# Kernel optimization log

Measured on AMD Instinct MI355X. Metric: run time of the kernel, lower is better.

## Reference

```python
import jax, jax.numpy as jnp
import numpy as np

OUTLINER_RATIO = 0.01
RANK = 16
SVD_NITER = 2  # matches torch.svd_lowrank default


def _randomized_svd(A, rank, key, niter=SVD_NITER):
    # torch.svd_lowrank-style randomized range finder + small SVD.
    n, d = A.shape
    Omega = jax.random.normal(key, (d, rank), dtype=A.dtype)
    Q, _ = jnp.linalg.qr(A @ Omega)               # [n, rank]
    for _ in range(niter):
        Q, _ = jnp.linalg.qr(A.T @ Q)             # [d, rank]
        Q, _ = jnp.linalg.qr(A @ Q)               # [n, rank]
    B = Q.T @ A                                   # [rank, d]
    Ub, S, Vh = jnp.linalg.svd(B, full_matrices=False)
    U = Q @ Ub                                    # [n, rank]
    return U, S, Vh


def get_statistics(x, outliner_ratio):
    # threshold such that ~outliner_ratio fraction of |x| exceeds it
    return jnp.quantile(jnp.abs(x), 1.0 - outliner_ratio)


def compress(x, outliner, rank, key):
    # split outliers (kept exactly) from sub-outlier part (low-rank compressed)
    x_outlier = jnp.where(jnp.abs(x) > outliner, x, jnp.zeros((), x.dtype))
    x_sub = (x - x_outlier).reshape(-1, x.shape[-1])   # [N, D]
    U, S, Vh = _randomized_svd(x_sub, rank, key)
    R = Vh.T                                           # [D, rank]
    Rinv = Vh                                          # orthonormal -> pinv = transpose
    L = x_sub @ R                                      # [N, rank]
    return x_outlier, L, R, Rinv


def reference(x, iteration):
    result = jax.nn.silu(x)
    # iteration < 10 branch: compute fresh outlier statistics
    outliner = get_statistics(x, OUTLINER_RATIO)
    # iteration % 50 == 0 -> execute_svd = True (iteration = 0 here)
    key = jax.random.key(42)
    x_outlier_compressed, L, R, Rinv = compress(x, outliner, RANK, key)
    return result, outliner, R, Rinv


def setup_inputs() -> dict:
    key = jax.random.key(0)
    x = jax.random.normal(key, (4, 2048, 4096), dtype=jnp.float32)
    return {"x": x, "iteration": 0}
```

## Files before the change

### kernel.cpp

```cpp
#include <hip/hip_runtime.h>
#include <math.h>


#define N_TOTAL 33554432
#define DDIM    4096
#define NROWS   8192
#define NCHUNK  32
#define RTARGET 33218888u

__device__ __forceinline__ double frcp(double x){
  double r = (double)(1.0f/(float)x);
  r = r*(2.0 - x*r);
  r = r*(2.0 - x*r);
  return r;
}
__device__ __forceinline__ double frsqrt(double x){
  double r = (double)rsqrtf((float)x);
  double hx = 0.5*x;
  r = r*(1.5 - hx*r*r);
  r = r*(1.5 - hx*r*r);
  return r;
}
__device__ __forceinline__ double fsqrt(double x){
  return (x == 0.0) ? 0.0 : x*frsqrt(x);
}
__device__ __forceinline__ double frcp1(double x){
  double r = (double)(1.0f/(float)x);
  r = r*(2.0 - x*r);
  return r;
}
__device__ __forceinline__ double frsqrt1(double x){
  double r = (double)rsqrtf((float)x);
  r = r*(1.5 - (0.5*x)*r*r);
  return r;
}
__device__ __forceinline__ double fsqrt1(double x){
  return (x == 0.0) ? 0.0 : x*frsqrt1(x);
}

__device__ __forceinline__ double dsign(double a, double b){ return (b >= 0.0) ? fabs(a) : -fabs(a); }

__device__ __forceinline__ void f_slartg(double f, double g, double& c, double& s, double& r){
  if (g == 0.0){ c=1.0; s=0.0; r=f; }
  else if (f == 0.0){ c=0.0; s=dsign(1.0,g); r=fabs(g); }
  else {
    double d2 = f*f+g*g;
    double inv = frsqrt1(d2);
    c = fabs(f)*inv;
    r = dsign(d2*inv, f);
    s = g*inv*dsign(1.0,f);
  }
}

__device__ void f_slas2(double f, double g, double h, double& ssmin, double& ssmax){
  double fa=fabs(f), ga=fabs(g), ha=fabs(h);
  double fhmn=fmin(fa,ha), fhmx=fmax(fa,ha);
  if (fhmn == 0.0){
    ssmin=0.0;
    if (fhmx==0.0) ssmax=ga;
    else { double mx=fmax(fhmx,ga), mn=fmin(fhmx,ga); double q=mn*frcp1(mx); ssmax = mx*fsqrt1(1.0+q*q); }
  } else {
    if (ga < fhmx){
      double rinv = frcp1(fhmx);
      double as_=1.0+fhmn*rinv, at=(fhmx-fhmn)*rinv, au=ga*rinv; au=au*au;
      double c=2.0*frcp1(fsqrt1(as_*as_+au)+fsqrt1(at*at+au));
      ssmin=fhmn*c; ssmax=fhmx*frcp1(c);
    } else {
      double au=fhmx*frcp1(ga);
      if (au==0.0){ ssmin=(fhmn*fhmx)*frcp1(ga); ssmax=ga; }
      else {
        double rinv = frcp1(fhmx);
        double as_=1.0+fhmn*rinv, at=(fhmx-fhmn)*rinv;
        double c=frcp1(fsqrt1(1.0+(as_*au)*(as_*au))+fsqrt1(1.0+(at*au)*(at*au)));
        ssmin=(fhmn*c)*au; ssmin=ssmin+ssmin; ssmax=ga*frcp1(c+c);
      }
    }
  }
}

__device__ void f_slasv2(double f, double g, double h,
                         double& ssmin, double& ssmax, double& snr, double& csr, double& snl, double& csl){
  const double EPSd = 5.9604645e-8;
  double ft=f, fa=fabs(f), ht=h, ha=fabs(h);
  int pmax=1;
  bool swap_=(ha>fa);
  if (swap_){ pmax=3; double t=ft; ft=ht; ht=t; t=fa; fa=ha; ha=t; }
  double gt=g, ga=fabs(g);
  double clt=0, crt=0, slt=0, srt=0;
  if (ga == 0.0){ ssmin=ha; ssmax=fa; clt=1; crt=1; slt=0; srt=0; }
  else {
    bool gasmal=true;
    if (ga > fa){
      pmax=2;
      if ((fa*frcp1(ga)) < EPSd){
        gasmal=false;
        ssmax=ga;
        ssmin = (ha>1.0) ? (fa*frcp1(ga*frcp1(ha))) : ((fa*frcp1(ga))*ha);
        clt=1; slt=ht*frcp1(gt); srt=1; crt=ft*frcp1(gt);
      }
    }
    if (gasmal){
      double d_=fa-ha;
      double fainv = frcp1(fa);
      double l_=(d_==fa)?1.0:(d_*fainv);
      double m_=gt*frcp1(ft);
      double t_=2.0-l_;
      double mm=m_*m_, tt=t_*t_;
      double s_=fsqrt1(tt+mm);
      double r_=(l_==0.0)?fabs(m_):fsqrt1(l_*l_+mm);
      double a_=0.5*(s_+r_);
      double ainv = frcp1(a_);
      ssmin=ha*ainv;
      ssmax=fa*a_;
      if (mm==0.0){
        t_=(l_==0.0)?(dsign(2.0,ft)*dsign(1.0,gt)):(gt*frcp1(dsign(d_,ft))+m_*frcp1(t_));
      } else {
        t_=(m_*frcp1(s_+t_)+m_*frcp1(r_+l_))*(1.0+a_);
      }
      l_=fsqrt1(t_*t_+4.0);
      double linv = frcp1(l_);
      crt=2.0*linv;
      srt=t_*linv;
      clt=(crt+srt*m_)*ainv;
      slt=(ht*frcp1(ft))*srt*ainv;
    }
  }
  if (swap_){ csl=srt; snl=crt; csr=slt; snr=clt; }
  else { csl=clt; snl=slt; csr=crt; snr=srt; }
  double tsign=0.0;
  if (pmax==1) tsign = dsign(1.0,csr)*dsign(1.0,csl)*dsign(1.0,f);
  if (pmax==2) tsign = dsign(1.0,snr)*dsign(1.0,csl)*dsign(1.0,g);
  if (pmax==3) tsign = dsign(1.0,snr)*dsign(1.0,snl)*dsign(1.0,h);
  ssmax = dsign(ssmax, tsign);
  ssmin = dsign(ssmin, tsign*dsign(1.0,f)*dsign(1.0,h));
}

__global__ __launch_bounds__(256) void k_hist1(const float4* __restrict__ x4, unsigned* __restrict__ h1){
  __shared__ unsigned lh[4096];
  for (int i=threadIdx.x; i<4096; i+=256) lh[i]=0u;
  __syncthreads();
  int tid = blockIdx.x*blockDim.x + threadIdx.x;
  int stride = gridDim.x*blockDim.x;
  for (int i = tid; i < N_TOTAL/4; i += stride){
    float4 v = x4[i];
    atomicAdd(&lh[(__float_as_uint(v.x)&0x7FFFFFFFu)>>19], 1u);
    atomicAdd(&lh[(__float_as_uint(v.y)&0x7FFFFFFFu)>>19], 1u);
    atomicAdd(&lh[(__float_as_uint(v.z)&0x7FFFFFFFu)>>19], 1u);
    atomicAdd(&lh[(__float_as_uint(v.w)&0x7FFFFFFFu)>>19], 1u);
  }
  __syncthreads();
  for (int i=threadIdx.x; i<4096; i+=256){ unsigned c=lh[i]; if (c) atomicAdd(&h1[i], c); }
}

__global__ __launch_bounds__(256) void k_siluhist(const float4* __restrict__ x4, float4* __restrict__ o4,
                                                  unsigned* __restrict__ h1){
  __shared__ unsigned lh[4096];
  for (int i=threadIdx.x; i<4096; i+=256) lh[i]=0u;
  __syncthreads();
  int tid = blockIdx.x*blockDim.x + threadIdx.x;
  int stride = gridDim.x*blockDim.x;
  for (int i = tid; i < N_TOTAL/4; i += stride){
    float4 v = x4[i];
    float4 o;
    o.x = v.x / (1.0f + expf(-v.x));
    o.y = v.y / (1.0f + expf(-v.y));
    o.z = v.z / (1.0f + expf(-v.z));
    o.w = v.w / (1.0f + expf(-v.w));
    o4[i] = o;
    atomicAdd(&lh[(__float_as_uint(v.x)&0x7FFFFFFFu)>>19], 1u);
    atomicAdd(&lh[(__float_as_uint(v.y)&0x7FFFFFFFu)>>19], 1u);
    atomicAdd(&lh[(__float_as_uint(v.z)&0x7FFFFFFFu)>>19], 1u);
    atomicAdd(&lh[(__float_as_uint(v.w)&0x7FFFFFFFu)>>19], 1u);
  }
  __syncthreads();
  for (int i=threadIdx.x; i<4096; i+=256){ unsigned c=lh[i]; if (c) atomicAdd(&h1[i], c); }
}

__global__ __launch_bounds__(1024) void k_select1(const unsigned* __restrict__ h1, unsigned* __restrict__ sel){
  __shared__ unsigned ssum[1024];
  int t = threadIdx.x;
  unsigned psum = 0;
  for (int k=0;k<4;++k) psum += h1[t*4+k];
  ssum[t]=psum; __syncthreads();
  for (int off=1; off<1024; off<<=1){
    unsigned v = (t>=off)? ssum[t-off]:0u;
    __syncthreads();
    ssum[t] += v;
    __syncthreads();
  }
  unsigned incl = ssum[t], excl = incl - psum;
  if (excl <= RTARGET && RTARGET < incl){
    unsigned run = excl;
    for (int k=0;k<4;++k){
      unsigned c = h1[t*4+k];
      if (run + c > RTARGET){ sel[1]=(unsigned)(t*4+k); sel[2]=RTARGET-run; break; }
      run += c;
    }
  }
}

__global__ void k_hist2(const float4* __restrict__ x4, unsigned* __restrict__ h2, const unsigned* __restrict__ sel){
  unsigned hstar = sel[1];
  int tid = blockIdx.x*blockDim.x + threadIdx.x;
  int stride = gridDim.x*blockDim.x;
  for (int i = tid; i < N_TOTAL/4; i += stride){
    float4 v = x4[i];
    unsigned b;
    b = __float_as_uint(v.x) & 0x7FFFFFFFu; if ((b>>19)==hstar) atomicAdd(&h2[b&0x7FFFFu],1u);
    b = __float_as_uint(v.y) & 0x7FFFFFFFu; if ((b>>19)==hstar) atomicAdd(&h2[b&0x7FFFFu],1u);
    b = __float_as_uint(v.z) & 0x7FFFFFFFu; if ((b>>19)==hstar) atomicAdd(&h2[b&0x7FFFFu],1u);
    b = __float_as_uint(v.w) & 0x7FFFFFFFu; if ((b>>19)==hstar) atomicAdd(&h2[b&0x7FFFFu],1u);
  }
}

__global__ __launch_bounds__(128) void k_grpsum(const uint4* __restrict__ h2v, unsigned* __restrict__ gs){
  __shared__ unsigned red[128];
  int g = blockIdx.x, t = threadIdx.x;
  uint4 v = h2v[(size_t)g*128 + t];
  red[t] = v.x+v.y+v.z+v.w;
  __syncthreads();
  for (int off=64; off; off>>=1){ if (t<off) red[t] += red[t+off]; __syncthreads(); }
  if (t==0) gs[g] = red[0];
}

__global__ __launch_bounds__(1024) void k_select2b(const unsigned* __restrict__ gs, const unsigned* __restrict__ h2,
                                                   unsigned* __restrict__ sel, float* __restrict__ outScalar){
  __shared__ unsigned ssum[1024];
  __shared__ unsigned sg[2];
  int t = threadIdx.x;
  unsigned target = sel[2], hstar = sel[1];
  unsigned psum = gs[t];
  ssum[t]=psum; __syncthreads();
  for (int off=1; off<1024; off<<=1){
    unsigned v = (t>=off)? ssum[t-off]:0u;
    __syncthreads();
    ssum[t] += v;
    __syncthreads();
  }
  unsigned incl = ssum[t], excl = incl - psum;
  if (excl <= target && target < incl){ sg[0]=(unsigned)t; sg[1]=excl; }
  __syncthreads();
  unsigned g = sg[0], gexcl = sg[1];
  unsigned cnt = (t<512) ? h2[(size_t)g*512 + t] : 0u;
  __syncthreads();
  ssum[t]=cnt; __syncthreads();
  for (int off=1; off<1024; off<<=1){
    unsigned v = (t>=off)? ssum[t-off]:0u;
    __syncthreads();
    ssum[t] += v;
    __syncthreads();
  }
  unsigned incl2 = ssum[t], excl2 = incl2 - cnt;
  unsigned rem = target - gexcl;
  if (t < 512 && excl2 <= rem && rem < incl2){
    unsigned tb = (hstar<<19) | (g*512 + (unsigned)t);
    float tv = __uint_as_float(tb);
    ((float*)sel)[0] = tv;
    *outScalar = tv;
  }
}

__device__ __forceinline__ unsigned rotl32(unsigned x, int r){ return (x<<r)|(x>>(32-r)); }

__device__ __forceinline__ float bits_to_normal(unsigned g){
  float u01 = __uint_as_float((g>>9) | 0x3F800000u) - 1.0f;
  float u = __fadd_rn(__fmul_rn(u01, 2.0f), -0.99999994f);
  u = fmaxf(-0.99999994f, u);
  float xx = __fmul_rn(u,u);
  float w = -log1pf(-xx);
  float p;
  if (w < 5.0f){
    w = __fadd_rn(w, -2.5f);
    p = 2.81022636e-08f;
    p = __fadd_rn(3.43273939e-07f, __fmul_rn(p,w));
    p = __fadd_rn(-3.5233877e-06f, __fmul_rn(p,w));
    p = __fadd_rn(-4.39150654e-06f, __fmul_rn(p,w));
    p = __fadd_rn(0.00021858087f, __fmul_rn(p,w));
    p = __fadd_rn(-0.00125372503f, __fmul_rn(p,w));
    p = __fadd_rn(-0.00417768164f, __fmul_rn(p,w));
    p = __fadd_rn(0.246640727f, __fmul_rn(p,w));
    p = __fadd_rn(1.50140941f, __fmul_rn(p,w));
  } else {
    w = __fadd_rn(sqrtf(w), -3.0f);
    p = -0.000200214257f;
    p = __fadd_rn(0.000100950558f, __fmul_rn(p,w));
    p = __fadd_rn(0.00134934322f, __fmul_rn(p,w));
    p = __fadd_rn(-0.00367342844f, __fmul_rn(p,w));
    p = __fadd_rn(0.00573950773f, __fmul_rn(p,w));
    p = __fadd_rn(-0.0076224613f, __fmul_rn(p,w));
    p = __fadd_rn(0.00943887047f, __fmul_rn(p,w));
    p = __fadd_rn(1.00167406f, __fmul_rn(p,w));
    p = __fadd_rn(2.83297682f, __fmul_rn(p,w));
  }
  return __fmul_rn(__uint_as_float(0x3FB504F3u), __fmul_rn(p,u));
}

#define TF_ROUND(r) { x0 += x1; x1 = rotl32(x1,(r)); x1 ^= x0; }

__global__ void k_omega(float* __restrict__ om){
  unsigned p = blockIdx.x*blockDim.x + threadIdx.x;
  unsigned x0 = p, x1 = 32768u + p;
  const unsigned ks0 = 0u, ks1 = 42u, ks2 = 0x1BD11BDAu ^ 0u ^ 42u;
  x0 += ks0; x1 += ks1;
  TF_ROUND(13) TF_ROUND(15) TF_ROUND(26) TF_ROUND(6)   x0+=ks1; x1+=ks2+1u;
  TF_ROUND(17) TF_ROUND(29) TF_ROUND(16) TF_ROUND(24)  x0+=ks2; x1+=ks0+2u;
  TF_ROUND(13) TF_ROUND(15) TF_ROUND(26) TF_ROUND(6)   x0+=ks0; x1+=ks1+3u;
  TF_ROUND(17) TF_ROUND(29) TF_ROUND(16) TF_ROUND(24)  x0+=ks1; x1+=ks2+4u;
  TF_ROUND(13) TF_ROUND(15) TF_ROUND(26) TF_ROUND(6)   x0+=ks2; x1+=ks0+5u;
  om[p]         = bits_to_normal(x0);
  om[p+32768u]  = bits_to_normal(x1);
}

__global__ __launch_bounds__(256) void k_gemmA(const float* __restrict__ x, const float* __restrict__ W,
                                               float* __restrict__ Y, const float* __restrict__ sel){
  __shared__ float xs[16][128];
  __shared__ float ws[128][16];
  const float t = sel[0];
  const int tid = threadIdx.x;
  const int c = tid & 15, rl = tid >> 4;
  const int row0 = blockIdx.x*16;
  const int c8 = c*8;
  const int wk = (tid*8) >> 4, wc = (tid*8) & 15;
  double acc = 0.0;
  for (int kt = 0; kt < DDIM; kt += 128){
    const float4* p = (const float4*)(x + (size_t)(row0+rl)*DDIM + kt + c8);
    float4 a = p[0], b = p[1];
    xs[rl][c8+0] = (fabsf(a.x) > t) ? 0.0f : a.x;
    xs[rl][c8+1] = (fabsf(a.y) > t) ? 0.0f : a.y;
    xs[rl][c8+2] = (fabsf(a.z) > t) ? 0.0f : a.z;
    xs[rl][c8+3] = (fabsf(a.w) > t) ? 0.0f : a.w;
    xs[rl][c8+4] = (fabsf(b.x) > t) ? 0.0f : b.x;
    xs[rl][c8+5] = (fabsf(b.y) > t) ? 0.0f : b.y;
    xs[rl][c8+6] = (fabsf(b.z) > t) ? 0.0f : b.z;
    xs[rl][c8+7] = (fabsf(b.w) > t) ? 0.0f : b.w;
    const float4* q = (const float4*)(W + (size_t)kt*16 + tid*8);
    float4 wa = q[0], wb = q[1];
    float* dstw = &ws[wk][wc];
    dstw[0]=wa.x; dstw[1]=wa.y; dstw[2]=wa.z; dstw[3]=wa.w;
    dstw[4]=wb.x; dstw[5]=wb.y; dstw[6]=wb.z; dstw[7]=wb.w;
    __syncthreads();
    #pragma unroll
    for (int k=0;k<128;k+=2){
      float2 xv2 = *(const float2*)&xs[rl][k];
      acc += (double)xv2.x*(double)ws[k][c];
      acc += (double)xv2.y*(double)ws[k+1][c];
    }
    __syncthreads();
  }
  Y[(size_t)(row0+rl)*16 + c] = (float)acc;
}

__global__ __launch_bounds__(256) void k_gemmAT(const float* __restrict__ x, const float* __restrict__ Q,
                                                double* __restrict__ part, const float* __restrict__ sel){
  __shared__ float qs[128][16];
  const float t = sel[0];
  const int tid = threadIdx.x;
  const int d = blockIdx.x*256 + tid;
  const int chunk = blockIdx.y;
  const int i0 = chunk*(NROWS/NCHUNK);
  double acc[16];
  #pragma unroll
  for (int c=0;c<16;++c) acc[c]=0.0;
  for (int it=0; it<NROWS/NCHUNK; it+=128){
    if (tid < 128){
      const float4* src = (const float4*)(Q + (size_t)(i0+it)*16) + tid*4;
      float4 a = src[0], b = src[1], c4 = src[2], d4 = src[3];
      float* dst = &qs[0][0] + tid*16;
      dst[0]=a.x; dst[1]=a.y; dst[2]=a.z; dst[3]=a.w;
      dst[4]=b.x; dst[5]=b.y; dst[6]=b.z; dst[7]=b.w;
      dst[8]=c4.x; dst[9]=c4.y; dst[10]=c4.z; dst[11]=c4.w;
      dst[12]=d4.x; dst[13]=d4.y; dst[14]=d4.z; dst[15]=d4.w;
    }
    __syncthreads();
    for (int ii=0; ii<128; ++ii){
      float xv = x[(size_t)(i0+it+ii)*DDIM + d];
      xv = (fabsf(xv) > t) ? 0.0f : xv;
      double xd = (double)xv;
      #pragma unroll
      for (int c2=0;c2<8;++c2){
        float2 q2 = *(const float2*)&qs[ii][c2*2];
        acc[c2*2]   += xd*(double)q2.x;
        acc[c2*2+1] += xd*(double)q2.y;
      }
    }
    __syncthreads();
  }
  double* pp = part + ((size_t)chunk*DDIM + d)*16;
  #pragma unroll
  for (int c=0;c<16;++c) pp[c]=acc[c];
}

__global__ void k_reduceT(const double* __restrict__ part, float* __restrict__ outM, int asB, int nchunks){
  int idx = blockIdx.x*blockDim.x + threadIdx.x;
  if (idx >= DDIM*16) return;
  double s = 0.0;
  for (int c=0;c<nchunks;++c) s += part[(size_t)c*DDIM*16 + idx];
  int d = idx >> 4, r = idx & 15;
  if (asB) outM[(size_t)r*DDIM + d] = (float)s;
  else     outM[idx] = (float)s;
}

__device__ void redchol_body(const double* part, int nchunks, double* Lout, double* Uinv,
                             double (*Gs)[17], double (*Vs)[17], int t){
  {
    double s = 0.0;
    for (int c=0;c<nchunks;++c) s += part[(size_t)c*256 + t];
    Gs[t>>4][t&15] = s;
  }
  __syncthreads();
  int l = t;
  for (int k=0;k<16;++k){
    if (l==k) Gs[k][k] = fsqrt(Gs[k][k]);
    __syncthreads();
    if (l>k && l<16) Gs[k][l] = Gs[k][l]*frcp(Gs[k][k]);
    __syncthreads();
    if (l>k && l<16){
      double g = Gs[k][l];
      for (int i=k+1;i<=l;++i) Gs[i][l] -= Gs[k][i]*g;
    }
    __syncthreads();
  }
  if (l<16){
    for (int i=0;i<16;++i) Vs[i][l] = 0.0;
    Vs[l][l] = frcp(Gs[l][l]);
    for (int i=l-1;i>=0;--i){
      double s = 0.0;
      for (int k=i+1;k<=l;++k) s += Gs[i][k]*Vs[k][l];
      Vs[i][l] = -s*frcp(Gs[i][i]);
    }
  }
  __syncthreads();
  if (l<16){
    for (int c=0;c<16;++c){
      Lout[l*16+c] = (c<=l) ? Gs[c][l] : 0.0;
      Uinv[l*16+c] = (l<=c) ? Vs[l][c] : 0.0;
    }
  }
}

__global__ __launch_bounds__(256) void k_gramMC(const float* __restrict__ M, int rowsPerChunk,
                                                double* __restrict__ part,
                                                double* __restrict__ Lout, double* __restrict__ Uinv,
                                                unsigned* __restrict__ ctr){
  __shared__ float lds[16][17];
  __shared__ double Gs[16][17];
  __shared__ double Vs[16][17];
  __shared__ unsigned slast;
  int t = threadIdx.x; int i = t>>4, j = t&15;
  int r0 = blockIdx.x*rowsPerChunk;
  double acc = 0.0;
  for (int rt=0; rt<rowsPerChunk; rt+=16){
    lds[t>>4][t&15] = M[(size_t)(r0+rt+(t>>4))*16 + (t&15)];
    __syncthreads();
    #pragma unroll
    for (int dd2=0; dd2<16; ++dd2) acc += (double)lds[dd2][i]*(double)lds[dd2][j];
    __syncthreads();
  }
  part[(size_t)blockIdx.x*256 + t] = acc;
  __threadfence();
  if (t==0) slast = atomicAdd(ctr, 1u);
  __syncthreads();
  if (slast != gridDim.x-1u) return;
  __threadfence();
  redchol_body(part, (int)gridDim.x, Lout, Uinv, Gs, Vs, t);
  __syncthreads();
  if (t==0) *ctr = 0u;
}

__global__ __launch_bounds__(256) void k_gramBC(const float* __restrict__ B,
                                                double* __restrict__ part,
                                                double* __restrict__ Lout, double* __restrict__ Uinv,
                                                unsigned* __restrict__ ctr){
  __shared__ float lds[16][17];
  __shared__ double Gs[16][17];
  __shared__ double Vs[16][17];
  __shared__ unsigned slast;
  int t = threadIdx.x; int i = t>>4, j = t&15;
  int d0 = blockIdx.x*256;
  double acc = 0.0;
  for (int dt=0; dt<256; dt+=16){
    lds[t>>4][t&15] = B[(size_t)(t>>4)*DDIM + d0+dt+(t&15)];
    __syncthreads();
    #pragma unroll
    for (int dd2=0; dd2<16; ++dd2) acc += (double)lds[i][dd2]*(double)lds[j][dd2];
    __syncthreads();
  }
  part[(size_t)blockIdx.x*256 + t] = acc;
  __threadfence();
  if (t==0) slast = atomicAdd(ctr, 1u);
  __syncthreads();
  if (slast != gridDim.x-1u) return;
  __threadfence();
  redchol_body(part, (int)gridDim.x, Lout, Uinv, Gs, Vs, t);
  __syncthreads();
  if (t==0) *ctr = 0u;
}

__global__ __launch_bounds__(256) void k_applyRinv(float* __restrict__ M, const double* __restrict__ Uinv){
  __shared__ double su[256];
  int t = threadIdx.x;
  su[t] = Uinv[t];
  int r = blockIdx.x*16 + (t>>4);
  int j = t & 15;
  const float4* rp = (const float4*)(M + (size_t)r*16);
  float4 v0=rp[0], v1=rp[1], v2=rp[2], v3=rp[3];
  float rowv[16] = {v0.x,v0.y,v0.z,v0.w, v1.x,v1.y,v1.z,v1.w,
                    v2.x,v2.y,v2.z,v2.w, v3.x,v3.y,v3.z,v3.w};
  __syncthreads();
  double acc = 0.0;
  #pragma unroll
  for (int k=0;k<16;++k) acc += (double)rowv[k]*su[k*16+j];
  M[(size_t)r*16 + j] = (float)acc;
}

__global__ __launch_bounds__(64) void k_smallsvd(const double* __restrict__ Lg, double* __restrict__ Wout){
  __shared__ double Lm[16][16];
  __shared__ double VT[16][16];
  __shared__ double A1[16][16];
  __shared__ double dd[16], ee[16], tp[16];
  __shared__ double csv[16], snv[16];
  int l = threadIdx.x;
  for (int idx=l; idx<256; idx+=64){ int r=idx>>4, c=idx&15; Lm[r][c] = (c<=r)? Lg[r*16+c] : 0.0; }
  __syncthreads();
  for (int i=0;i<16;++i){
    double xn2=0.0;
    for (int r=i+1;r<16;++r){ double v=Lm[r][i]; xn2 += v*v; }
    double alpha = Lm[i][i];
    double beta, tauq_, scl;
    if (xn2==0.0){ tauq_=0.0; beta=alpha; scl=0.0; }
    else { beta = -dsign(fsqrt1(alpha*alpha+xn2), alpha); tauq_=(beta-alpha)*frcp1(beta); scl=frcp1(alpha-beta); }
    __syncthreads();
    if (l>i && l<16) Lm[l][i] *= scl;
    __syncthreads();
    dd[i]=beta;
    if (tauq_ != 0.0 && l>i && l<16){
      int j=l;
      double w = Lm[i][j];
      for (int r=i+1;r<16;++r) w += Lm[r][i]*Lm[r][j];
      w *= tauq_;
      Lm[i][j] -= w;
      for (int r=i+1;r<16;++r) Lm[r][j] -= w*Lm[r][i];
    }
    __syncthreads();
    if (i<15){
      double xn2b=0.0;
      for (int c=i+2;c<16;++c){ double v=Lm[i][c]; xn2b+=v*v; }
      double alpha2=Lm[i][i+1];
      double beta2, taup_, scl2;
      if (xn2b==0.0){ taup_=0.0; beta2=alpha2; scl2=0.0; }
      else { beta2=-dsign(fsqrt1(alpha2*alpha2+xn2b),alpha2); taup_=(beta2-alpha2)*frcp1(beta2); scl2=frcp1(alpha2-beta2); }
      __syncthreads();
      if (l>=i+2 && l<16) Lm[i][l] *= scl2;
      __syncthreads();
      ee[i]=beta2; tp[i]=taup_;
      if (taup_!=0.0 && l>i && l<16){
        int r=l;
        double w=Lm[r][i+1];
        for (int c=i+2;c<16;++c) w += Lm[i][c]*Lm[r][c];
        w *= taup_;
        Lm[r][i+1] -= w;
        for (int c=i+2;c<16;++c) Lm[r][c] -= w*Lm[i][c];
      }
      __syncthreads();
    } else { tp[i]=0.0; __syncthreads(); }
  }
  for (int idx=l; idx<256; idx+=64){ int r=idx>>4,c=idx&15; VT[r][c]=(r==c)?1.0:0.0; }
  __syncthreads();
  const double EPSs = 5.9604645e-8;
  const double UNFL = 1.17549435e-38;
  double tol = 10.0*EPSs;
  double sminoa, mu;
  sminoa = mu = fabs(dd[0]);
  if (sminoa != 0.0){
    for (int k=1;k<16;++k){ mu = fabs(dd[k])*(mu*frcp1(mu+fabs(ee[k-1]))); sminoa=fmin(sminoa,mu); if (sminoa==0.0) break; }
  }
  sminoa = sminoa/4.0;
  double thresh = fmax(tol*sminoa, 6.0*16.0*16.0*UNFL);
  int m=16, oldll=-1, oldm=-1, idir=0;
  double sminl=0.0;
  int guard=0;
  #define Dv(k) dd[(k)-1]
  #define Ev(k) ee[(k)-1]
  while (m > 1 && guard < 3000){
    ++guard;
    int ll=0; bool split=false;
    double smax_=fabs(Dv(m)), smin_=smax_;
    for (int lll=1; lll<=m-1; ++lll){
      ll = m-lll;
      double abss=fabs(Dv(ll)), abse=fabs(Ev(ll));
      if (abse <= thresh){ split=true; break; }
      smin_=fmin(smin_,abss); smax_=fmax(smax_,fmax(abss,abse));
    }
    if (!split) ll=0;
    else {
      Ev(ll)=0.0;
      if (ll == m-1){ m = m-1; continue; }
    }
    ll = ll+1;
    if (ll == m-1){
      double sigmn,sigmx,sinr,cosr,sinl_,cosl;
      f_slasv2(Dv(m-1), Ev(m-1), Dv(m), sigmn, sigmx, sinr, cosr, sinl_, cosl);
      Dv(m-1)=sigmx; Ev(m-1)=0.0; Dv(m)=sigmn;
      if (l<16){
        double t0 = cosr*VT[m-2][l] + sinr*VT[m-1][l];
        VT[m-1][l] = cosr*VT[m-1][l] - sinr*VT[m-2][l];
        VT[m-2][l] = t0;
      }
      __syncthreads();
      m -= 2; continue;
    }
    if (ll > oldm || m < oldll) idir = (fabs(Dv(ll)) >= fabs(Dv(m))) ? 1 : 2;
    bool cont=false;
    if (idir==1){
      if (fabs(Ev(m-1)) <= tol*fabs(Dv(m))){ Ev(m-1)=0.0; continue; }
      mu = fabs(Dv(ll)); sminl=mu;
      for (int lll=ll; lll<=m-1; ++lll){
        if (fabs(Ev(lll)) <= tol*mu){ Ev(lll)=0.0; cont=true; break; }
        mu = fabs(Dv(lll+1))*(mu*frcp1(mu+fabs(Ev(lll)))); sminl=fmin(sminl,mu);
      }
    } else {
      if (fabs(Ev(ll)) <= tol*fabs(Dv(ll))){ Ev(ll)=0.0; continue; }
      mu = fabs(Dv(m)); sminl=mu;
      for (int lll=m-1; lll>=ll; --lll){
        if (fabs(Ev(lll)) <= tol*mu){ Ev(lll)=0.0; cont=true; break; }
        mu = fabs(Dv(lll))*(mu*frcp1(mu+fabs(Ev(lll)))); sminl=fmin(sminl,mu);
      }
    }
    if (cont) continue;
    oldll=ll; oldm=m;
    double shift=0.0, rdum;
    if (!( 16.0*tol*(sminl*frcp1(smax_)) <= fmax(EPSs, 0.01*tol) )){
      double sll;
      if (idir==1){ sll=fabs(Dv(ll)); f_slas2(Dv(m-1), Ev(m-1), Dv(m), shift, rdum); }
      else        { sll=fabs(Dv(m));  f_slas2(Dv(ll), Ev(ll), Dv(ll+1), shift, rdum); }
      if (sll>0.0){ double q=shift*frcp1(sll); if (q*q < EPSs) shift=0.0; }
    }
    if (shift == 0.0){
      if (idir==1){
        double cs=1.0, oldcs=1.0, oldsn=0.0, r_;
        double dcur = Dv(ll);
        for (int i1=ll;i1<=m-1;++i1){
          double cn, snn;
          double a0 = dcur*cs;
          f_slartg(a0, Ev(i1), cn, snn, r_);
          if (i1>ll) Ev(i1-1) = oldsn*r_;
          double dnx = Dv(i1+1);
          double ocn, osn, dnew;
          f_slartg(oldcs*r_, dnx*snn, ocn, osn, dnew);
          Dv(i1)=dnew;
          cs=cn; oldcs=ocn; oldsn=osn;
          csv[i1-1]=cs; snv[i1-1]=snn;
          dcur = dnx;
        }
        double h=dcur*cs;
        Dv(m)=h*oldcs; Ev(m-1)=h*oldsn;
        if (fabs(Ev(m-1))<=thresh) Ev(m-1)=0.0;
        __syncthreads();
        if (l<16){
          double v = VT[ll-1][l];
          for (int i1=ll;i1<=m-1;++i1){
            double c=csv[i1-1], s=snv[i1-1];
            double w = VT[i1][l];
            VT[i1-1][l] = c*v + s*w;
            v = c*w - s*v;
          }
          VT[m-1][l] = v;
        }
      } else {
        double cs=1.0, oldcs=1.0, oldsn=0.0, r_;
        double dcur = Dv(m);
        for (int i1=m;i1>=ll+1;--i1){
          double cn,snn;
          double a0 = dcur*cs;
          f_slartg(a0, Ev(i1-1), cn, snn, r_);
          if (i1<m) Ev(i1)=oldsn*r_;
          double dnx = Dv(i1-1);
          double ocn,osn,dnew;
          f_slartg(oldcs*r_, dnx*snn, ocn, osn, dnew);
          Dv(i1)=dnew;
          cs=cn; oldcs=ocn; oldsn=osn;
          csv[i1-2]=oldcs; snv[i1-2]=-oldsn;
          dcur = dnx;
        }
        double h=dcur*cs;
        Dv(ll)=h*oldcs; Ev(ll)=h*oldsn;
        if (fabs(Ev(ll))<=thresh) Ev(ll)=0.0;
        __syncthreads();
        if (l<16){
          double v = VT[m-1][l];
          for (int i1=m;i1>=ll+1;--i1){
            double c=csv[i1-2], s=snv[i1-2];
            double w = VT[i1-2][l];
            VT[i1-1][l] = c*v - s*w;
            v = c*w + s*v;
          }
          VT[ll-1][l] = v;
        }
      }
    } else {
      if (idir==1){
        double f=(fabs(Dv(ll))-shift)*(dsign(1.0,Dv(ll))+shift*frcp1(Dv(ll)));
        double g=Ev(ll);
        double dcur = Dv(ll), ecur = Ev(ll);
        double r_;
        for (int i1=ll;i1<=m-1;++i1){
          double cosr,sinr,cosl,sinl_;
          double dnx = Dv(i1+1);
          f_slartg(f,g,cosr,sinr,r_);
          if (i1>ll) Ev(i1-1)=r_;
          f = cosr*dcur + sinr*ecur;
          double e_mid = cosr*ecur - sinr*dcur;
          g = sinr*dnx;
          double d_mid = cosr*dnx;
          f_slartg(f,g,cosl,sinl_,r_);
          Dv(i1)=r_;
          f = cosl*e_mid + sinl_*d_mid;
          double d_fin = cosl*d_mid - sinl_*e_mid;
          double e_fin = 0.0;
          if (i1 < m-1){ double enx = Ev(i1+1); g = sinl_*enx; e_fin = cosl*enx; }
          csv[i1-1]=cosr; snv[i1-1]=sinr;
          dcur = d_fin; ecur = e_fin;
        }
        Dv(m) = dcur;
        Ev(m-1)=f;
        if (fabs(Ev(m-1))<=thresh) Ev(m-1)=0.0;
        __syncthreads();
        if (l<16){
          double v = VT[ll-1][l];
          for (int i1=ll;i1<=m-1;++i1){
            double c=csv[i1-1], s=snv[i1-1];
            double w = VT[i1][l];
            VT[i1-1][l] = c*v + s*w;
            v = c*w - s*v;
          }
          VT[m-1][l] = v;
        }
      } else {
        double f=(fabs(Dv(m))-shift)*(dsign(1.0,Dv(m))+shift*frcp1(Dv(m)));
        double g=Ev(m-1);
        double dcur = Dv(m), ecur = Ev(m-1);
        double r_;
        for (int i1=m;i1>=ll+1;--i1){
          double cosr,sinr,cosl,sinl_;
          double dnx = Dv(i1-1);
          f_slartg(f,g,cosr,sinr,r_);
          if (i1<m) Ev(i1)=r_;
          f = cosr*dcur + sinr*ecur;
          double e_mid = cosr*ecur - sinr*dcur;
          g = sinr*dnx;
          double d_mid = cosr*dnx;
          f_slartg(f,g,cosl,sinl_,r_);
          Dv(i1)=r_;
          f = cosl*e_mid + sinl_*d_mid;
          double d_fin = cosl*d_mid - sinl_*e_mid;
          double e_fin = 0.0;
          if (i1 > ll+1){ double enx = Ev(i1-2); g = sinl_*enx; e_fin = cosl*enx; }
          csv[i1-2]=cosr; snv[i1-2]=-sinr;
          dcur = d_fin; ecur = e_fin;
        }
        Dv(ll) = dcur;
        Ev(ll)=f;
        if (fabs(Ev(ll))<=thresh) Ev(ll)=0.0;
        __syncthreads();
        if (l<16){
          double v = VT[m-1][l];
          for (int i1=m;i1>=ll+1;--i1){
            double c=csv[i1-2], s=snv[i1-2];
            double w = VT[i1-2][l];
            VT[i1-1][l] = c*v - s*w;
            v = c*w + s*v;
          }
          VT[ll-1][l] = v;
        }
      }
    }
    __syncthreads();
  }
  __syncthreads();
  for (int k=1;k<=16;++k){
    if (Dv(k) < 0.0){
      Dv(k) = -Dv(k);
      if (l<16) VT[k-1][l] = -VT[k-1][l];
    }
    __syncthreads();
  }
  for (int i1=1;i1<=15;++i1){
    int isub=1; double smn=Dv(1);
    for (int j=2;j<=17-i1;++j){ if (Dv(j) <= smn){ isub=j; smn=Dv(j);} }
    if (isub != 17-i1){
      double tmpd = Dv(17-i1);
      __syncthreads();
      Dv(isub)=tmpd; Dv(17-i1)=smn;
      if (l<16){ double t2=VT[isub-1][l]; VT[isub-1][l]=VT[16-i1][l]; VT[16-i1][l]=t2; }
    }
    __syncthreads();
  }
  for (int i=14;i>=0;--i){
    double tpv = tp[i];
    if (tpv != 0.0 && l<16){
      int r=l;
      double w = VT[r][i+1];
      for (int c=i+2;c<16;++c) w += VT[r][c]*Lm[i][c];
      w *= tpv;
      VT[r][i+1] -= w;
      for (int c=i+2;c<16;++c) VT[r][c] -= w*Lm[i][c];
    }
    __syncthreads();
  }
  if (l<16){
    int r=l;
    for (int j=15;j>=0;--j){
      double s = VT[r][j];
      for (int k=j+1;k<16;++k) s -= A1[r][k]*Lg[k*16+j];
      A1[r][j] = s*frcp1(Lg[j*16+j]);
    }
    for (int j=0;j<16;++j) Wout[r*16+j] = A1[r][j];
  }
  #undef Dv
  #undef Ev
}

__global__ __launch_bounds__(256) void k_formVh2(const float* __restrict__ B, const double* __restrict__ W,
                                                 float* __restrict__ outR, float* __restrict__ outRinv){
  __shared__ double sW[256];
  int t = threadIdx.x;
  sW[t] = W[t];
  __syncthreads();
  int d = blockIdx.x*256 + t;
  double bi[16];
  #pragma unroll
  for (int i=0;i<16;++i) bi[i] = (double)B[(size_t)i*DDIM + d];
  #pragma unroll
  for (int r=0;r<16;++r){
    double s = 0.0;
    #pragma unroll
    for (int i=0;i<16;++i) s += sW[r*16+i]*bi[i];
    float f = (float)s;
    outRinv[(size_t)r*DDIM + d] = f;
    outR[(size_t)d*16 + r] = f;
  }
}

__global__ void k_silu(const float4* __restrict__ x4, float4* __restrict__ o4){
  int tid = blockIdx.x*blockDim.x + threadIdx.x;
  int stride = gridDim.x*blockDim.x;
  for (int i = tid; i < N_TOTAL/4; i += stride){
    float4 v = x4[i];
    float4 o;
    o.x = v.x / (1.0f + expf(-v.x));
    o.y = v.y / (1.0f + expf(-v.y));
    o.z = v.z / (1.0f + expf(-v.z));
    o.w = v.w / (1.0f + expf(-v.w));
    o4[i] = o;
  }
}

static void cholQR(float* M, int N, double* partG, double* Ld, double* Uinvd, unsigned* ctr,
                   hipStream_t stream){
  k_gramMC<<<32,256,0,stream>>>(M, N/32, partG, Ld, Uinvd, ctr);
  k_applyRinv<<<N/16,256,0,stream>>>(M, Uinvd);
}

extern "C" void kernel_launch(void* const* d_in, const int* in_sizes, int n_in,
                              void* d_out, int out_size, void* d_ws, size_t ws_size,
                              hipStream_t stream) {
  (void)in_sizes; (void)n_in; (void)out_size;
  const float* x = (const float*)d_in[0];
  float* out = (float*)d_out;
  const size_t NEEDED = 20512832;
  const bool useWs = (d_ws != nullptr) && (ws_size >= NEEDED);
  float* scr = useWs ? (float*)d_ws : out;
  unsigned* h1   = (unsigned*)scr;
  unsigned* h2   = (unsigned*)(scr + 4096);
  unsigned* ctr  = (unsigned*)(scr + 528384);
  unsigned* selu = (unsigned*)(scr + 528400);
  float*    self = (float*)selu;
  unsigned* gs   = (unsigned*)(scr + 528496);
  float* Om = scr + 532496;
  float* Y  = scr + 598032;
  float* T  = scr + 729104;
  float* B  = scr + 794640;
  double* dsm  = (double*)(scr + 860192);
  double* Ld   = dsm;
  double* Uinvd= dsm + 256;
  double* Wd   = dsm + 512;
  double* part = (double*)(scr + 917520);
  double* partG= (double*)(scr + 5111824);
  float* outScalar = out + (size_t)N_TOTAL;
  float* outR      = out + (size_t)N_TOTAL + 1;
  float* outRinv   = out + (size_t)N_TOTAL + 1 + 65536;

  hipMemsetAsync(h1, 0, (4096+524288+16)*sizeof(unsigned), stream);
  if (useWs){
    k_siluhist<<<2048,256,0,stream>>>((const float4*)x, (float4*)out, h1);
  } else {
    k_hist1<<<1024,256,0,stream>>>((const float4*)x, h1);
  }
  k_select1<<<1,1024,0,stream>>>(h1, selu);
  k_hist2<<<2048,256,0,stream>>>((const float4*)x, h2, selu);
  k_grpsum<<<1024,128,0,stream>>>((const uint4*)h2, gs);
  k_select2b<<<1,1024,0,stream>>>(gs, h2, selu, outScalar);
  k_omega<<<128,256,0,stream>>>(Om);

  k_gemmA<<<512,256,0,stream>>>(x, Om, Y, self);
  cholQR(Y, NROWS, partG, Ld, Uinvd, ctr, stream);
  for (int it=0; it<2; ++it){
    k_gemmAT<<<dim3(16,NCHUNK),256,0,stream>>>(x, Y, part, self);
    k_reduceT<<<256,256,0,stream>>>(part, T, 0, NCHUNK);
    cholQR(T, DDIM, partG, Ld, Uinvd, ctr, stream);
    k_gemmA<<<512,256,0,stream>>>(x, T, Y, self);
    cholQR(Y, NROWS, partG, Ld, Uinvd, ctr, stream);
  }
  k_gemmAT<<<dim3(16,NCHUNK),256,0,stream>>>(x, Y, part, self);
  k_reduceT<<<256,256,0,stream>>>(part, B, 1, NCHUNK);
  k_gramBC<<<16,256,0,stream>>>(B, partG, Ld, Uinvd, ctr);
  k_smallsvd<<<1,64,0,stream>>>(Ld, Wd);
  k_formVh2<<<16,256,0,stream>>>(B, Wd, outR, outRinv);
  if (!useWs){
    k_silu<<<2048,256,0,stream>>>((const float4*)x, (float4*)out);
  }
}
```

Baseline: 1.090 ms.

## Fold Cholesky-QR R-inverse into GEMM loads and fuse partial reduction with Gram

Removes the separate applyRinv passes by having the next GEMM kernel apply the 16x16 inverse-R factor to its operand tile while loading it into shared memory. Also merges the chunk-partial reduction (reduceT) into the following Gram/Cholesky kernel, so the reduced T or B is written and its Gram partial computed in one kernel. This cuts several small kernel launches and extra global round trips per iteration. The cost is redundant 16x16 matmul work per tile and fewer blocks (32 or 16) doing the partial reduction. Y and T are now stored unnormalized, and the normalization is applied lazily.

```diff
diff --git a/kernel.cpp b/kernel.cpp
--- a/kernel.cpp
+++ b/kernel.cpp
@@ -312,15 +312,19 @@
 }
 
 __global__ __launch_bounds__(256) void k_gemmA(const float* __restrict__ x, const float* __restrict__ W,
-                                               float* __restrict__ Y, const float* __restrict__ sel){
+                                               float* __restrict__ Y, const float* __restrict__ sel,
+                                               const double* __restrict__ UinvG, int applyU){
   __shared__ float xs[16][128];
   __shared__ float ws[128][16];
+  __shared__ double su[256];
   const float t = sel[0];
   const int tid = threadIdx.x;
   const int c = tid & 15, rl = tid >> 4;
   const int row0 = blockIdx.x*16;
   const int c8 = c*8;
   const int wk = (tid*8) >> 4, wc = (tid*8) & 15;
+  if (applyU) su[tid] = UinvG[tid];
+  __syncthreads();
   double acc = 0.0;
   for (int kt = 0; kt < DDIM; kt += 128){
     const float4* p = (const float4*)(x + (size_t)(row0+rl)*DDIM + kt + c8);
@@ -333,11 +337,26 @@
     xs[rl][c8+5] = (fabsf(b.y) > t) ? 0.0f : b.y;
     xs[rl][c8+6] = (fabsf(b.z) > t) ? 0.0f : b.z;
     xs[rl][c8+7] = (fabsf(b.w) > t) ? 0.0f : b.w;
-    const float4* q = (const float4*)(W + (size_t)kt*16 + tid*8);
-    float4 wa = q[0], wb = q[1];
-    float* dstw = &ws[wk][wc];
-    dstw[0]=wa.x; dstw[1]=wa.y; dstw[2]=wa.z; dstw[3]=wa.w;
-    dstw[4]=wb.x; dstw[5]=wb.y; dstw[6]=wb.z; dstw[7]=wb.w;
+    if (applyU){
+      const float* trow = W + (size_t)(kt+wk)*16;
+      const float4* t4 = (const float4*)trow;
+      float4 ta=t4[0], tb=t4[1], tc=t4[2], td=t4[3];
+      float tv[16] = {ta.x,ta.y,ta.z,ta.w, tb.x,tb.y,tb.z,tb.w,
+                      tc.x,tc.y,tc.z,tc.w, td.x,td.y,td.z,td.w};
+      #pragma unroll
+      for (int jj=0;jj<8;++jj){
+        double s2 = 0.0;
+        #pragma unroll
+        for (int k2=0;k2<16;++k2) s2 += (double)tv[k2]*su[k2*16 + wc+jj];
+        ws[wk][wc+jj] = (float)s2;
+      }
+    } else {
+      const float4* q = (const float4*)(W + (size_t)kt*16 + tid*8);
+      float4 wa = q[0], wb = q[1];
+      float* dstw = &ws[wk][wc];
+      dstw[0]=wa.x; dstw[1]=wa.y; dstw[2]=wa.z; dstw[3]=wa.w;
+      dstw[4]=wb.x; dstw[5]=wb.y; dstw[6]=wb.z; dstw[7]=wb.w;
+    }
     __syncthreads();
     #pragma unroll
     for (int k=0;k<128;k+=2){
@@ -351,25 +370,33 @@
 }
 
 __global__ __launch_bounds__(256) void k_gemmAT(const float* __restrict__ x, const float* __restrict__ Q,
+                                                const double* __restrict__ UinvG,
                                                 double* __restrict__ part, const float* __restrict__ sel){
   __shared__ float qs[128][16];
+  __shared__ double su[256];
   const float t = sel[0];
   const int tid = threadIdx.x;
   const int d = blockIdx.x*256 + tid;
   const int chunk = blockIdx.y;
   const int i0 = chunk*(NROWS/NCHUNK);
+  su[tid] = UinvG[tid];
+  __syncthreads();
   double acc[16];
   #pragma unroll
   for (int c=0;c<16;++c) acc[c]=0.0;
   for (int it=0; it<NROWS/NCHUNK; it+=128){
     if (tid < 128){
-      const float4* src = (const float4*)(Q + (size_t)(i0+it)*16) + tid*4;
+      const float4* src = (const float4*)(Q + (size_t)(i0+it+tid)*16);
       float4 a = src[0], b = src[1], c4 = src[2], d4 = src[3];
-      float* dst = &qs[0][0] + tid*16;
-      dst[0]=a.x; dst[1]=a.y; dst[2]=a.z; dst[3]=a.w;
-      dst[4]=b.x; dst[5]=b.y; dst[6]=b.z; dst[7]=b.w;
-      dst[8]=c4.x; dst[9]=c4.y; dst[10]=c4.z; dst[11]=c4.w;
-      dst[12]=d4.x; dst[13]=d4.y; dst[14]=d4.z; dst[15]=d4.w;
+      float yv[16] = {a.x,a.y,a.z,a.w, b.x,b.y,b.z,b.w,
+                      c4.x,c4.y,c4.z,c4.w, d4.x,d4.y,d4.z,d4.w};
+      #pragma unroll
+      for (int jj=0;jj<16;++jj){
+        double s2 = 0.0;
+        #pragma unroll
+        for (int k2=0;k2<16;++k2) s2 += (double)yv[k2]*su[k2*16 + jj];
+        qs[tid][jj] = (float)s2;
+      }
     }
     __syncthreads();
     for (int ii=0; ii<128; ++ii){
@@ -388,16 +415,6 @@
   double* pp = part + ((size_t)chunk*DDIM + d)*16;
   #pragma unroll
   for (int c=0;c<16;++c) pp[c]=acc[c];
-}
-
-__global__ void k_reduceT(const double* __restrict__ part, float* __restrict__ outM, int asB, int nchunks){
-  int idx = blockIdx.x*blockDim.x + threadIdx.x;
-  if (idx >= DDIM*16) return;
-  double s = 0.0;
-  for (int c=0;c<nchunks;++c) s += part[(size_t)c*DDIM*16 + idx];
-  int d = idx >> 4, r = idx & 15;
-  if (asB) outM[(size_t)r*DDIM + d] = (float)s;
-  else     outM[idx] = (float)s;
 }
 
 __device__ void redchol_body(const double* part, int nchunks, double* Lout, double* Uinv,
@@ -467,50 +484,81 @@
   if (t==0) *ctr = 0u;
 }
 
-__global__ __launch_bounds__(256) void k_gramBC(const float* __restrict__ B,
-                                                double* __restrict__ part,
+__global__ __launch_bounds__(256) void k_gramTR(const double* __restrict__ part, float* __restrict__ T,
+                                                double* __restrict__ partG,
                                                 double* __restrict__ Lout, double* __restrict__ Uinv,
                                                 unsigned* __restrict__ ctr){
-  __shared__ float lds[16][17];
+  __shared__ float sT[128][17];
   __shared__ double Gs[16][17];
   __shared__ double Vs[16][17];
   __shared__ unsigned slast;
   int t = threadIdx.x; int i = t>>4, j = t&15;
-  int d0 = blockIdx.x*256;
+  int b = blockIdx.x;
+  #pragma unroll
+  for (int e=0;e<8;++e){
+    int idx = t + e*256;
+    int row = idx >> 4, col = idx & 15;
+    size_t gidx = ((size_t)(b*128 + row))*16 + col;
+    double s = 0.0;
+    for (int c=0;c<NCHUNK;++c) s += part[(size_t)c*DDIM*16 + gidx];
+    float v = (float)s;
+    sT[row][col] = v;
+    T[gidx] = v;
+  }
+  __syncthreads();
+  double acc = 0.0;
+  for (int rt=0; rt<128; rt+=16){
+    #pragma unroll
+    for (int dd2=0; dd2<16; ++dd2) acc += (double)sT[rt+dd2][i]*(double)sT[rt+dd2][j];
+  }
+  partG[(size_t)b*256 + t] = acc;
+  __threadfence();
+  if (t==0) slast = atomicAdd(ctr, 1u);
+  __syncthreads();
+  if (slast != gridDim.x-1u) return;
+  __threadfence();
+  redchol_body(partG, (int)gridDim.x, Lout, Uinv, Gs, Vs, t);
+  __syncthreads();
+  if (t==0) *ctr = 0u;
+}
+
+__global__ __launch_bounds__(256) void k_gramBR(const double* __restrict__ part, float* __restrict__ B,
+                                                double* __restrict__ partG,
+                                                double* __restrict__ Lout, double* __restrict__ Uinv,
+                                                unsigned* __restrict__ ctr){
+  __shared__ float sB[16][257];
+  __shared__ double Gs[16][17];
+  __shared__ double Vs[16][17];
+  __shared__ unsigned slast;
+  int t = threadIdx.x; int i = t>>4, j = t&15;
+  int b = blockIdx.x; int d0 = b*256;
+  #pragma unroll
+  for (int e=0;e<16;++e){
+    int idx = t + e*256;
+    int r = idx >> 8;
+    int dl = idx & 255;
+    size_t gidx = ((size_t)(d0+dl))*16 + r;
+    double s = 0.0;
+    for (int c=0;c<NCHUNK;++c) s += part[(size_t)c*DDIM*16 + gidx];
+    float v = (float)s;
+    sB[r][dl] = v;
+    B[(size_t)r*DDIM + d0+dl] = v;
+  }
+  __syncthreads();
   double acc = 0.0;
   for (int dt=0; dt<256; dt+=16){
-    lds[t>>4][t&15] = B[(size_t)(t>>4)*DDIM + d0+dt+(t&15)];
-    __syncthreads();
     #pragma unroll
-    for (int dd2=0; dd2<16; ++dd2) acc += (double)lds[i][dd2]*(double)lds[j][dd2];
-    __syncthreads();
-  }
-  part[(size_t)blockIdx.x*256 + t] = acc;
+    for (int dd2=0; dd2<16; ++dd2) acc += (double)sB[i][dt+dd2]*(double)sB[j][dt+dd2];
+  }
+  partG[(size_t)b*256 + t] = acc;
   __threadfence();
   if (t==0) slast = atomicAdd(ctr, 1u);
   __syncthreads();
   if (slast != gridDim.x-1u) return;
   __threadfence();
-  redchol_body(part, (int)gridDim.x, Lout, Uinv, Gs, Vs, t);
+  redchol_body(partG, (int)gridDim.x, Lout, Uinv, Gs, Vs, t);
   __syncthreads();
   if (t==0) *ctr = 0u;
-}
-
-__global__ __launch_bounds__(256) void k_applyRinv(float* __restrict__ M, const double* __restrict__ Uinv){
-  __shared__ double su[256];
-  int t = threadIdx.x;
-  su[t] = Uinv[t];
-  int r = blockIdx.x*16 + (t>>4);
-  int j = t & 15;
-  const float4* rp = (const float4*)(M + (size_t)r*16);
-  float4 v0=rp[0], v1=rp[1], v2=rp[2], v3=rp[3];
-  float rowv[16] = {v0.x,v0.y,v0.z,v0.w, v1.x,v1.y,v1.z,v1.w,
-                    v2.x,v2.y,v2.z,v2.w, v3.x,v3.y,v3.z,v3.w};
-  __syncthreads();
-  double acc = 0.0;
-  #pragma unroll
-  for (int k=0;k<16;++k) acc += (double)rowv[k]*su[k*16+j];
-  M[(size_t)r*16 + j] = (float)acc;
 }
 
 __global__ __launch_bounds__(64) void k_smallsvd(const double* __restrict__ Lg, double* __restrict__ Wout){
@@ -855,12 +903,6 @@
   }
 }
 
-static void cholQR(float* M, int N, double* partG, double* Ld, double* Uinvd, unsigned* ctr,
-                   hipStream_t stream){
-  k_gramMC<<<32,256,0,stream>>>(M, N/32, partG, Ld, Uinvd, ctr);
-  k_applyRinv<<<N/16,256,0,stream>>>(M, Uinvd);
-}
-
 extern "C" void kernel_launch(void* const* d_in, const int* in_sizes, int n_in,
                               void* d_out, int out_size, void* d_ws, size_t ws_size,
                               hipStream_t stream) {
@@ -902,18 +944,16 @@
   k_select2b<<<1,1024,0,stream>>>(gs, h2, selu, outScalar);
   k_omega<<<128,256,0,stream>>>(Om);
 
-  k_gemmA<<<512,256,0,stream>>>(x, Om, Y, self);
-  cholQR(Y, NROWS, partG, Ld, Uinvd, ctr, stream);
+  k_gemmA<<<512,256,0,stream>>>(x, Om, Y, self, Uinvd, 0);
+  k_gramMC<<<32,256,0,stream>>>(Y, NROWS/32, partG, Ld, Uinvd, ctr);
   for (int it=0; it<2; ++it){
-    k_gemmAT<<<dim3(16,NCHUNK),256,0,stream>>>(x, Y, part, self);
-    k_reduceT<<<256,256,0,stream>>>(part, T, 0, NCHUNK);
-    cholQR(T, DDIM, partG, Ld, Uinvd, ctr, stream);
-    k_gemmA<<<512,256,0,stream>>>(x, T, Y, self);
-    cholQR(Y, NROWS, partG, Ld, Uinvd, ctr, stream);
-  }
-  k_gemmAT<<<dim3(16,NCHUNK),256,0,stream>>>(x, Y, part, self);
-  k_reduceT<<<256,256,0,stream>>>(part, B, 1, NCHUNK);
-  k_gramBC<<<16,256,0,stream>>>(B, partG, Ld, Uinvd, ctr);
+    k_gemmAT<<<dim3(16,NCHUNK),256,0,stream>>>(x, Y, Uinvd, part, self);
+    k_gramTR<<<32,256,0,stream>>>(part, T, partG, Ld, Uinvd, ctr);
+    k_gemmA<<<512,256,0,stream>>>(x, T, Y, self, Uinvd, 1);
+    k_gramMC<<<32,256,0,stream>>>(Y, NROWS/32, partG, Ld, Uinvd, ctr);
+  }
+  k_gemmAT<<<dim3(16,NCHUNK),256,0,stream>>>(x, Y, Uinvd, part, self);
+  k_gramBR<<<16,256,0,stream>>>(part, B, partG, Ld, Uinvd, ctr);
   k_smallsvd<<<1,64,0,stream>>>(Ld, Wd);
   k_formVh2<<<16,256,0,stream>>>(B, Wd, outR, outRinv);
   if (!useWs){
```

New measurement: 1.147 ms. 5.2% more time.
